# Kernel optimization log

Measured on AMD Instinct MI355X. Metric: run time of the kernel, lower is better.

Reference implementation:

```python
import jax, jax.numpy as jnp
import numpy as np

ALPHA = 0.1


def setup_inputs() -> dict:
    key = jax.random.key(0)
    ks = jax.random.split(key, 6)
    N, D, K = 512, 128, 16  # yad_num, embedding_dim, co-occurrence list width
    x = jax.random.randint(ks[0], (N, K), 0, N)
    wid_pos_mu = jax.random.normal(ks[1], (N, D), dtype=jnp.float32)
    ken_pos_mu = jax.random.normal(ks[2], (N, D), dtype=jnp.float32)
    lrg_pos_mu = jax.random.normal(ks[3], (N, D), dtype=jnp.float32)
    sml_pos_mu = jax.random.normal(ks[4], (N, D), dtype=jnp.float32)
    yad_pos = jax.random.normal(ks[5], (N, D), dtype=jnp.float32)
    return {
        "wid_pos_mu": wid_pos_mu,
        "ken_pos_mu": ken_pos_mu,
        "lrg_pos_mu": lrg_pos_mu,
        "sml_pos_mu": sml_pos_mu,
        "yad_pos": yad_pos,
        "x": x,
    }


def _loss(wid_pos_mu, ken_pos_mu, lrg_pos_mu, sml_pos_mu, yad_pos, x):
    # Hierarchical consistency term (elementwise, requires equal table sizes
    # exactly as the torch code does).
    loss = (
        jnp.sum((wid_pos_mu - ken_pos_mu) ** 2)
        + jnp.sum((wid_pos_mu - lrg_pos_mu) ** 2)
        + jnp.sum((lrg_pos_mu - sml_pos_mu) ** 2)
        + jnp.sum((sml_pos_mu - yad_pos) ** 2)
    )

    N = yad_pos.shape[0]
    # Membership mask M[i, j] = (j in x[i])
    M = jnp.zeros((N, N), dtype=bool).at[jnp.arange(N)[:, None], x].set(True)
    eye = jnp.eye(N, dtype=bool)
    pos = M & ~eye          # j in x[i], j != i
    neg = (~M) & ~eye       # k not in x[i], k != i  (j != k is implied)

    # Pairwise squared distances D2[i, j] = ||yad_i - yad_j||^2 via Gram trick
    sq = jnp.sum(yad_pos * yad_pos, axis=-1)                    # [N]
    gram = yad_pos @ yad_pos.T                                   # [N, N]
    D2 = sq[:, None] + sq[None, :] - 2.0 * gram                  # [N, N]

    # Triplet hinge over all valid (i, j, k): relu(d(i,j) - d(i,k) + alpha)
    T = D2[:, :, None] - D2[:, None, :] + ALPHA                  # [N, N, N]
    valid = pos[:, :, None] & neg[:, None, :]                    # [N, N, N]
    loss = loss + jnp.sum(jnp.where(valid, jax.nn.relu(T), 0.0))
    return loss


def reference(wid_pos_mu, ken_pos_mu, lrg_pos_mu, sml_pos_mu, yad_pos, x):
    return _loss(wid_pos_mu, ken_pos_mu, lrg_pos_mu, sml_pos_mu, yad_pos, x)
```

## Files before the change

kernel.cpp:

```cpp
#include <hip/hip_runtime.h>

constexpr int NN = 512;
constexpr int DD = 128;
constexpr int KK = 16;
#define ALPHA 0.1f

__global__ __launch_bounds__(256) void area_loss_kernel(
    const float* __restrict__ wid,
    const float* __restrict__ ken,
    const float* __restrict__ lrg,
    const float* __restrict__ sml,
    const float* __restrict__ yad,
    const int*   __restrict__ x,
    float* __restrict__ partial)
{
    __shared__ float    yi[DD];
    __shared__ float    d2[NN];
    __shared__ unsigned mask[NN / 32];
    __shared__ float    posd[KK];
    __shared__ int      pcnt;
    __shared__ float    wsum[4];

    const int i = blockIdx.x;
    const int t = threadIdx.x;

    if (t < DD)      yi[t]   = yad[(size_t)i * DD + t];
    if (t < NN / 32) mask[t] = 0u;
    if (t == 0)      pcnt    = 0;
    __syncthreads();

    if (t < KK) {
        int j = x[i * KK + t];
        atomicOr(&mask[j >> 5], 1u << (j & 31));
    }

    for (int j = t; j < NN; j += 256) {
        const float4* row = (const float4*)(yad + (size_t)j * DD);
        float acc = 0.f;
#pragma unroll
        for (int c = 0; c < DD / 4; ++c) {
            float4 v = row[c];
            float e0 = v.x - yi[4 * c + 0];
            float e1 = v.y - yi[4 * c + 1];
            float e2 = v.z - yi[4 * c + 2];
            float e3 = v.w - yi[4 * c + 3];
            acc += e0 * e0 + e1 * e1 + e2 * e2 + e3 * e3;
        }
        d2[j] = acc;
    }
    __syncthreads();

    for (int j = t; j < NN; j += 256) {
        if (j != i && ((mask[j >> 5] >> (j & 31)) & 1u)) {
            int p = atomicAdd(&pcnt, 1);
            posd[p] = d2[j];
        }
    }
    __syncthreads();

    const int P = pcnt;
    float acc = 0.f;

    for (int k = t; k < NN; k += 256) {
        if (k != i && !((mask[k >> 5] >> (k & 31)) & 1u)) {
            float dk = d2[k];
            for (int p = 0; p < P; ++p) {
                acc += fmaxf(posd[p] - dk + ALPHA, 0.f);
            }
        }
    }

    if (t < DD) {
        size_t idx = (size_t)i * DD + t;
        float w = wid[idx], kk = ken[idx], l = lrg[idx], s = sml[idx], y = yi[t];
        float a = w - kk, b = w - l, c = l - s, e = s - y;
        acc += a * a + b * b + c * c + e * e;
    }

    for (int off = 32; off; off >>= 1) acc += __shfl_down(acc, off, 64);
    if ((t & 63) == 0) wsum[t >> 6] = acc;
    __syncthreads();
    if (t == 0) {
        partial[i] = wsum[0] + wsum[1] + wsum[2] + wsum[3];
    }
}

__global__ __launch_bounds__(512) void reduce_kernel(
    const float* __restrict__ partial, float* __restrict__ out)
{
    __shared__ float wsum[8];
    const int t = threadIdx.x;
    float acc = partial[t];
    for (int off = 32; off; off >>= 1) acc += __shfl_down(acc, off, 64);
    if ((t & 63) == 0) wsum[t >> 6] = acc;
    __syncthreads();
    if (t == 0) {
        float s = 0.f;
#pragma unroll
        for (int w = 0; w < 8; ++w) s += wsum[w];
        out[0] = s;
    }
}

extern "C" void kernel_launch(void* const* d_in, const int* in_sizes, int n_in,
                              void* d_out, int out_size, void* d_ws, size_t ws_size,
                              hipStream_t stream) {
    const float* wid = (const float*)d_in[0];
    const float* ken = (const float*)d_in[1];
    const float* lrg = (const float*)d_in[2];
    const float* sml = (const float*)d_in[3];
    const float* yad = (const float*)d_in[4];
    const int*   x   = (const int*)d_in[5];
    float* out     = (float*)d_out;
    float* partial = (float*)d_ws;

    area_loss_kernel<<<NN, 256, 0, stream>>>(wid, ken, lrg, sml, yad, x, partial);
    reduce_kernel<<<1, NN, 0, stream>>>(partial, out);
}
```

Before: 82.19 us.

## Fuse final reduction via flag handoff and process two anchor rows per block

```diff
diff --git a/kernel.cpp b/kernel.cpp
--- a/kernel.cpp
+++ b/kernel.cpp
@@ -3,102 +3,141 @@
 constexpr int NN = 512;
 constexpr int DD = 128;
 constexpr int KK = 16;
+constexpr int GG = 2;
+constexpr int NB = NN / GG;
+constexpr int NT = 512;
 #define ALPHA 0.1f
+#define MAGIC 0x5CA1AB1Eu
 
-__global__ __launch_bounds__(256) void area_loss_kernel(
+__global__ __launch_bounds__(NT) void area_loss_fused(
     const float* __restrict__ wid,
     const float* __restrict__ ken,
     const float* __restrict__ lrg,
     const float* __restrict__ sml,
     const float* __restrict__ yad,
     const int*   __restrict__ x,
-    float* __restrict__ partial)
+    float*       __restrict__ out,
+    float*       __restrict__ partial,
+    unsigned*    __restrict__ flags)
 {
-    __shared__ float    yi[DD];
-    __shared__ float    d2[NN];
-    __shared__ unsigned mask[NN / 32];
-    __shared__ float    posd[KK];
-    __shared__ int      pcnt;
-    __shared__ float    wsum[4];
+    __shared__ float    yi[GG][DD];
+    __shared__ float    d2[GG][NN];
+    __shared__ unsigned mask[GG][NN / 32];
+    __shared__ int      xl[GG][KK];
+    __shared__ float    posd[GG][KK];
+    __shared__ int      pcnt[GG];
+    __shared__ float    wsum[NT / 64];
 
-    const int i = blockIdx.x;
+    const int b = blockIdx.x;
     const int t = threadIdx.x;
+    const int ibase = b * GG;
 
-    if (t < DD)      yi[t]   = yad[(size_t)i * DD + t];
-    if (t < NN / 32) mask[t] = 0u;
-    if (t == 0)      pcnt    = 0;
+    if (t < GG * DD)      ((float*)yi)[t]   = yad[(size_t)ibase * DD + t];
+    if (t < GG * NN / 32) ((unsigned*)mask)[t] = 0u;
+    if (t < GG * KK)      ((int*)xl)[t]     = x[ibase * KK + t];
+    if (t < GG)           pcnt[t] = 0;
     __syncthreads();
 
-    if (t < KK) {
-        int j = x[i * KK + t];
-        atomicOr(&mask[j >> 5], 1u << (j & 31));
+    if (t < GG * KK) {
+        int a = t / KK;
+        int j = xl[a][t % KK];
+        atomicOr(&mask[a][j >> 5], 1u << (j & 31));
     }
 
-    for (int j = t; j < NN; j += 256) {
-        const float4* row = (const float4*)(yad + (size_t)j * DD);
-        float acc = 0.f;
+    {
+        const float4* row = (const float4*)(yad + (size_t)t * DD);
+        float a0 = 0.f, a1 = 0.f;
 #pragma unroll
         for (int c = 0; c < DD / 4; ++c) {
             float4 v = row[c];
-            float e0 = v.x - yi[4 * c + 0];
-            float e1 = v.y - yi[4 * c + 1];
-            float e2 = v.z - yi[4 * c + 2];
-            float e3 = v.w - yi[4 * c + 3];
-            acc += e0 * e0 + e1 * e1 + e2 * e2 + e3 * e3;
+            float e;
+            e = v.x - yi[0][4 * c + 0]; a0 += e * e;
+            e = v.y - yi[0][4 * c + 1]; a0 += e * e;
+            e = v.z - yi[0][4 * c + 2]; a0 += e * e;
+            e = v.w - yi[0][4 * c + 3]; a0 += e * e;
+            e = v.x - yi[1][4 * c + 0]; a1 += e * e;
+            e = v.y - yi[1][4 * c + 1]; a1 += e * e;
+            e = v.z - yi[1][4 * c + 2]; a1 += e * e;
+            e = v.w - yi[1][4 * c + 3]; a1 += e * e;
         }
-        d2[j] = acc;
+        d2[0][t] = a0;
+        d2[1][t] = a1;
     }
     __syncthreads();
 
-    for (int j = t; j < NN; j += 256) {
-        if (j != i && ((mask[j >> 5] >> (j & 31)) & 1u)) {
-            int p = atomicAdd(&pcnt, 1);
-            posd[p] = d2[j];
+    if (t < GG * KK) {
+        int a = t / KK, e = t % KK;
+        int j = xl[a][e];
+        bool ok = (j != ibase + a);
+        for (int q = 0; q < e && ok; ++q)
+            if (xl[a][q] == j) ok = false;
+        if (ok) {
+            int p = atomicAdd(&pcnt[a], 1);
+            posd[a][p] = d2[a][j];
         }
     }
     __syncthreads();
 
-    const int P = pcnt;
     float acc = 0.f;
 
-    for (int k = t; k < NN; k += 256) {
-        if (k != i && !((mask[k >> 5] >> (k & 31)) & 1u)) {
-            float dk = d2[k];
-            for (int p = 0; p < P; ++p) {
-                acc += fmaxf(posd[p] - dk + ALPHA, 0.f);
-            }
+#pragma unroll
+    for (int a = 0; a < GG; ++a) {
+        const int ia = ibase + a;
+        const int P  = pcnt[a];
+        if (t != ia && !((mask[a][t >> 5] >> (t & 31)) & 1u)) {
+            float dk = d2[a][t];
+            for (int p = 0; p < P; ++p)
+                acc += fmaxf(posd[a][p] - dk + ALPHA, 0.f);
         }
     }
 
-    if (t < DD) {
-        size_t idx = (size_t)i * DD + t;
-        float w = wid[idx], kk = ken[idx], l = lrg[idx], s = sml[idx], y = yi[t];
-        float a = w - kk, b = w - l, c = l - s, e = s - y;
-        acc += a * a + b * b + c * c + e * e;
+    if (t < GG * DD) {
+        size_t idx = (size_t)ibase * DD + t;
+        float w = wid[idx], kk = ken[idx], l = lrg[idx], s = sml[idx];
+        float y = ((float*)yi)[t];
+        float p0 = w - kk, p1 = w - l, p2 = l - s, p3 = s - y;
+        acc += p0 * p0 + p1 * p1 + p2 * p2 + p3 * p3;
     }
 
     for (int off = 32; off; off >>= 1) acc += __shfl_down(acc, off, 64);
     if ((t & 63) == 0) wsum[t >> 6] = acc;
     __syncthreads();
-    if (t == 0) {
-        partial[i] = wsum[0] + wsum[1] + wsum[2] + wsum[3];
-    }
-}
 
-__global__ __launch_bounds__(512) void reduce_kernel(
-    const float* __restrict__ partial, float* __restrict__ out)
-{
-    __shared__ float wsum[8];
-    const int t = threadIdx.x;
-    float acc = partial[t];
-    for (int off = 32; off; off >>= 1) acc += __shfl_down(acc, off, 64);
-    if ((t & 63) == 0) wsum[t >> 6] = acc;
-    __syncthreads();
-    if (t == 0) {
-        float s = 0.f;
+    if (b != 0) {
+        if (t == 0) {
+            float s = 0.f;
 #pragma unroll
-        for (int w = 0; w < 8; ++w) s += wsum[w];
-        out[0] = s;
+            for (int w = 0; w < NT / 64; ++w) s += wsum[w];
+            partial[b] = s;
+            __hip_atomic_store(&flags[b], MAGIC, __ATOMIC_RELEASE,
+                               __HIP_MEMORY_SCOPE_AGENT);
+        }
+    } else {
+        float mine = 0.f;
+        if (t == 0) {
+#pragma unroll
+            for (int w = 0; w < NT / 64; ++w) mine += wsum[w];
+        }
+        __syncthreads();
+
+        float other = 0.f;
+        if (t >= 1 && t < NB) {
+            while (__hip_atomic_load(&flags[t], __ATOMIC_ACQUIRE,
+                                     __HIP_MEMORY_SCOPE_AGENT) != MAGIC) {
+                __builtin_amdgcn_s_sleep(1);
+            }
+            other = partial[t];
+        }
+        float tot = mine + other;
+        for (int off = 32; off; off >>= 1) tot += __shfl_down(tot, off, 64);
+        if ((t & 63) == 0) wsum[t >> 6] = tot;
+        __syncthreads();
+        if (t == 0) {
+            float s = 0.f;
+#pragma unroll
+            for (int w = 0; w < NT / 64; ++w) s += wsum[w];
+            out[0] = s;
+        }
     }
 }
 
@@ -111,9 +150,10 @@
     const float* sml = (const float*)d_in[3];
     const float* yad = (const float*)d_in[4];
     const int*   x   = (const int*)d_in[5];
-    float* out     = (float*)d_out;
-    float* partial = (float*)d_ws;
+    float*    out     = (float*)d_out;
+    float*    partial = (float*)d_ws;
+    unsigned* flags   = (unsigned*)(partial + NB);
 
-    area_loss_kernel<<<NN, 256, 0, stream>>>(wid, ken, lrg, sml, yad, x, partial);
-    reduce_kernel<<<1, NN, 0, stream>>>(partial, out);
+    area_loss_fused<<<NB, NT, 0, stream>>>(wid, ken, lrg, sml, yad, x,
+                                           out, partial, flags);
 }
```

Result: faster. 77.79 us (-5.4%).
